# Performance work log

Measured on AMD Instinct MI355X. Metric: run time of the kernel, lower is better.

The kernel has to match this reference:

```python
import jax, jax.numpy as jnp
import numpy as np

B, T, D, H, FF, E = 4, 1024, 1024, 16, 4096, 8
HD = D // H
EPS = 1e-5


def layernorm(x, g, b):
    mu = jnp.mean(x, axis=-1, keepdims=True)
    var = jnp.mean(jnp.square(x - mu), axis=-1, keepdims=True)
    return (x - mu) * jax.lax.rsqrt(var + EPS) * g + b


def setup_inputs() -> dict:
    key = jax.random.key(0)
    ks = jax.random.split(key, 24)
    s = 0.02
    inp = {
        "src": jax.random.normal(ks[0], (B, T, D), jnp.float32),
        "frac": jax.random.uniform(ks[1], (B, T), jnp.float32),
        "Wq": jax.random.normal(ks[2], (D, D), jnp.float32) * s,
        "bq": jnp.zeros((D,), jnp.float32),
        "Wk": jax.random.normal(ks[3], (D, D), jnp.float32) * s,
        "bk": jnp.zeros((D,), jnp.float32),
        "Wv": jax.random.normal(ks[4], (D, D), jnp.float32) * s,
        "bv": jnp.zeros((D,), jnp.float32),
        "Wo": jax.random.normal(ks[5], (D, D), jnp.float32) * s,
        "bo": jnp.zeros((D,), jnp.float32),
        "alpha_pos": jax.random.normal(ks[6], (H,), jnp.float32) * s,
        "alpha_neg": jax.random.normal(ks[7], (H,), jnp.float32) * s,
        "gate_W": jax.random.normal(ks[8], (D, E), jnp.float32) * s,
        "gate_b": jnp.zeros((E,), jnp.float32),
        "W1": jax.random.normal(ks[9], (E, D, FF), jnp.float32) * s,
        "b1": jnp.zeros((E, FF), jnp.float32),
        "W2": jax.random.normal(ks[10], (E, FF, D), jnp.float32) * s,
        "b2": jnp.zeros((E, D), jnp.float32),
        "ln1_g": jnp.ones((D,), jnp.float32),
        "ln1_b": jnp.zeros((D,), jnp.float32),
        "ln2_g": jnp.ones((D,), jnp.float32),
        "ln2_b": jnp.zeros((D,), jnp.float32),
    }
    return inp


def reference(src, frac, Wq, bq, Wk, bk, Wv, bv, Wo, bo, alpha_pos, alpha_neg,
              gate_W, gate_b, W1, b1, W2, b2, ln1_g, ln1_b, ln2_g, ln2_b):
    # ---- attention with per-head stoichiometric bias ----
    q = (src @ Wq + bq).reshape(B, T, H, HD).transpose(0, 2, 1, 3)  # [B,H,T,hd]
    k = (src @ Wk + bk).reshape(B, T, H, HD).transpose(0, 2, 1, 3)
    v = (src @ Wv + bv).reshape(B, T, H, HD).transpose(0, 2, 1, 3)
    scale = HD ** -0.5
    scores = jnp.einsum('bhqd,bhkd->bhqk', q, k) * scale  # [B,H,T,T]
    Dm = frac[:, None, :] - frac[:, :, None]  # frac_j - frac_i, [B,T,T]
    bias = (alpha_pos[None, :, None, None] * jax.nn.relu(Dm)[:, None]
            - alpha_neg[None, :, None, None] * jax.nn.relu(-Dm)[:, None])
    probs = jax.nn.softmax(scores + bias, axis=-1)
    attn = jnp.einsum('bhqk,bhkd->bhqd', probs, v)
    attn = attn.transpose(0, 2, 1, 3).reshape(B, T, D) @ Wo + bo

    x = layernorm(src + attn, ln1_g, ln1_b)

    # ---- top-2 MoE FFN ----
    logits = x @ gate_W + gate_b  # [B,T,E]
    gscores = jax.nn.softmax(logits, axis=-1)
    top2_scores, top2_idx = jax.lax.top_k(gscores, 2)  # [B,T,2]
    # dense per-expert combine weight: score if expert in top-2 else 0
    weights = jnp.sum(jax.nn.one_hot(top2_idx, E, dtype=x.dtype)
                      * top2_scores[..., None], axis=-2)  # [B,T,E]
    ff = jnp.zeros_like(x)
    for e in range(E):  # small fixed expert count
        h = jax.nn.relu(x @ W1[e] + b1[e])
        ff = ff + weights[..., e:e + 1] * (h @ W2[e] + b2[e])

    return layernorm(x + ff, ln2_g, ln2_b)
```

## Files before the change

kernel.cpp:

```cpp
#include <hip/hip_runtime.h>
#include <stdint.h>

typedef unsigned short u16;
typedef unsigned int   u32;

using bf16x8 = __attribute__((ext_vector_type(8))) short;
using f32x4  = __attribute__((ext_vector_type(4))) float;

#define N_T   1024
#define N_D   1024
#define N_E   8
#define N_BT  4096
#define LNEPS 1e-5f

__device__ __forceinline__ u32 rne2(float a, float b) {
  u32 ua = __float_as_uint(a); ua = (ua + 0x7fffu + ((ua >> 16) & 1u)) >> 16;
  u32 ub = __float_as_uint(b); ub = (ub + 0x7fffu + ((ub >> 16) & 1u)) >> 16;
  return ua | (ub << 16);
}
__device__ __forceinline__ u16 rne1(float a) {
  u32 ua = __float_as_uint(a);
  return (u16)((ua + 0x7fffu + ((ua >> 16) & 1u)) >> 16);
}
__device__ __forceinline__ float bfhi_f(float a) {
  u32 ua = __float_as_uint(a);
  ua = (ua + 0x7fffu + ((ua >> 16) & 1u)) & 0xffff0000u;
  return __uint_as_float(ua);
}
__device__ __forceinline__ int fch(int row) { return (row & 3) ^ ((row >> 2) & 3); }
__device__ __forceinline__ int swz(int row, int chunk) {
  return row * 32 + (((chunk ^ fch(row)) & 3) << 3);
}
__device__ __forceinline__ float wred(float v) {
  #pragma unroll
  for (int o2 = 32; o2 > 0; o2 >>= 1) v += __shfl_xor(v, o2, 64);
  return v;
}
__device__ __forceinline__ f32x4 mfma16(bf16x8 a, bf16x8 b, f32x4 c) {
  return __builtin_amdgcn_mfma_f32_16x16x32_bf16(a, b, c, 0, 0, 0);
}
typedef __attribute__((address_space(1))) const u32 gas_u32;
typedef __attribute__((address_space(3))) u32 las_u32;
__device__ __forceinline__ void gl16(const void* g, void* l) {
  __builtin_amdgcn_global_load_lds((gas_u32*)g, (las_u32*)l, 16, 0, 0);
}

template<int SPLIT>
__global__ __launch_bounds__(256)
void transpose_bf16(const float* __restrict__ in, u16* __restrict__ outh,
                    u16* __restrict__ outl, int R, int C, float scale)
{
  __shared__ u16 th[64][68];
  __shared__ u16 tl[SPLIT ? 64 : 1][SPLIT ? 68 : 1];
  const long long zb = (long long)blockIdx.z * R * C;
  const float* srcp = in + zb;
  const int r0 = blockIdx.y * 64, c0 = blockIdx.x * 64;
  const int t = threadIdx.x;
  {
    const int rr = t >> 4, cc = (t & 15) << 2;
    #pragma unroll
    for (int i = 0; i < 4; i++) {
      const int r = rr + i * 16;
      float4 v = *(const float4*)(srcp + (long long)(r0 + r) * C + c0 + cc);
      v.x *= scale; v.y *= scale; v.z *= scale; v.w *= scale;
      if constexpr (SPLIT) {
        float hx = bfhi_f(v.x), hy = bfhi_f(v.y), hz = bfhi_f(v.z), hw = bfhi_f(v.w);
        *(uint2*)&th[r][cc] = make_uint2(rne2(hx, hy), rne2(hz, hw));
        *(uint2*)&tl[r][cc] = make_uint2(rne2(v.x - hx, v.y - hy), rne2(v.z - hz, v.w - hw));
      } else {
        *(uint2*)&th[r][cc] = make_uint2(rne2(v.x, v.y), rne2(v.z, v.w));
      }
    }
  }
  __syncthreads();
  {
    const int c = t >> 2, rs = (t & 3) << 4;
    const long long ob = zb + (long long)(c0 + c) * R + r0 + rs;
    u32 w[8];
    #pragma unroll
    for (int i = 0; i < 8; i++)
      w[i] = (u32)th[rs + 2*i][c] | ((u32)th[rs + 2*i + 1][c] << 16);
    *(uint4*)(outh + ob)     = make_uint4(w[0], w[1], w[2], w[3]);
    *(uint4*)(outh + ob + 8) = make_uint4(w[4], w[5], w[6], w[7]);
    if constexpr (SPLIT) {
      #pragma unroll
      for (int i = 0; i < 8; i++)
        w[i] = (u32)tl[rs + 2*i][c] | ((u32)tl[rs + 2*i + 1][c] << 16);
      *(uint4*)(outl + ob)     = make_uint4(w[0], w[1], w[2], w[3]);
      *(uint4*)(outl + ob + 8) = make_uint4(w[4], w[5], w[6], w[7]);
    }
  }
}

__global__ __launch_bounds__(256)
void bias_cat(const float* __restrict__ bq, const float* __restrict__ bk,
              const float* __restrict__ bv, float* __restrict__ bcat)
{
  const int i = blockIdx.x * 256 + threadIdx.x;
  if (i < 1024)       bcat[i] = bq[i] * 0.125f;
  else if (i < 2048)  bcat[i] = bk[i - 1024];
  else if (i < 3072)  bcat[i] = bv[i - 2048];
}

__global__ __launch_bounds__(256)
void vtrans_bf16(const u16* __restrict__ Vh, const u16* __restrict__ Vl, int ldv,
                 u16* __restrict__ Vth, u16* __restrict__ Vtl)
{
  __shared__ u16 th[64][72];
  __shared__ u16 tl[64][72];
  const int bh = blockIdx.y, b = bh >> 4, h = bh & 15;
  const int kt = blockIdx.x, tid = threadIdx.x;
  {
    const int sr = tid >> 2, scb = (tid & 3) << 4;
    const long long off = (long long)(b * N_T + kt * 64 + sr) * ldv + h * 64 + scb;
    const uint4* vh = (const uint4*)(Vh + off);
    const uint4* vl = (const uint4*)(Vl + off);
    *(uint4*)&th[sr][scb]     = vh[0];
    *(uint4*)&th[sr][scb + 8] = vh[1];
    *(uint4*)&tl[sr][scb]     = vl[0];
    *(uint4*)&tl[sr][scb + 8] = vl[1];
  }
  __syncthreads();
  {
    const int od = tid >> 2, os0 = (tid & 3) << 4;
    u16 wh[16], wl[16];
    #pragma unroll
    for (int i = 0; i < 16; i++) { wh[i] = th[os0 + i][od]; wl[i] = tl[os0 + i][od]; }
    u16* oph = Vth + (long long)(bh * 64 + od) * N_T + kt * 64 + os0;
    u16* opl = Vtl + (long long)(bh * 64 + od) * N_T + kt * 64 + os0;
    *(uint4*)oph = make_uint4((u32)wh[0] | ((u32)wh[1] << 16), (u32)wh[2] | ((u32)wh[3] << 16),
                              (u32)wh[4] | ((u32)wh[5] << 16), (u32)wh[6] | ((u32)wh[7] << 16));
    *(uint4*)(oph + 8) = make_uint4((u32)wh[8] | ((u32)wh[9] << 16), (u32)wh[10] | ((u32)wh[11] << 16),
                                    (u32)wh[12] | ((u32)wh[13] << 16), (u32)wh[14] | ((u32)wh[15] << 16));
    *(uint4*)opl = make_uint4((u32)wl[0] | ((u32)wl[1] << 16), (u32)wl[2] | ((u32)wl[3] << 16),
                              (u32)wl[4] | ((u32)wl[5] << 16), (u32)wl[6] | ((u32)wl[7] << 16));
    *(uint4*)(opl + 8) = make_uint4((u32)wl[8] | ((u32)wl[9] << 16), (u32)wl[10] | ((u32)wl[11] << 16),
                                    (u32)wl[12] | ((u32)wl[13] << 16), (u32)wl[14] | ((u32)wl[15] << 16));
  }
}

template<int ASPLIT, int GATHER, int DORELU, int DOSCALE, int OBF, int GROUPED, int BSPL>
__global__ __launch_bounds__(256, 2)
void gemm128(const void* __restrict__ Ap, int lda,
             const u16* __restrict__ Bhp, const u16* __restrict__ Blp,
             long long bstride,
             void* __restrict__ Cp, int ldc,
             const float* __restrict__ biasp, int bias_stride,
             const float* __restrict__ slot_wp,
             const int* __restrict__ tokidx,
             const int2* __restrict__ tilesp, const int* __restrict__ ntilesp,
             int Ksz, void* __restrict__ Cp2, float cscale)
{
  const int gx = gridDim.x, nwg = gx * gridDim.y;
  const int orig = blockIdx.y * gx + blockIdx.x;
  const int qq = nwg >> 3, rr8 = nwg & 7;
  const int xcd = orig & 7, slot = orig >> 3;
  const int flat = (xcd < rr8 ? xcd * (qq + 1) : rr8 * (qq + 1) + (xcd - rr8) * qq) + slot;
  const int bxx = flat % gx, byy = flat / gx;

  int e = 0, row0;
  if constexpr (GROUPED) {
    if (bxx >= *ntilesp) return;
    const int2 dsc = tilesp[bxx];
    e = dsc.x; row0 = dsc.y;
  } else {
    row0 = bxx * 128;
  }
  const int col0 = byy * 128;

  __shared__ __align__(16) u16 AhS[128 * 32];
  __shared__ __align__(16) u16 BhS[128 * 32];
  __shared__ __align__(16) u16 AlS[ASPLIT ? 128 * 32 : 8];
  __shared__ __align__(16) u16 BlS[BSPL ? 128 * 32 : 8];

  const int tid = threadIdx.x, wid = tid >> 6, lane = tid & 63;
  const int wm = (wid >> 1) << 6, wn = (wid & 1) << 6;
  const int l15 = lane & 15, l4 = lane >> 4;

  const int srow0 = wid * 32 + (lane >> 2);
  const int srow1 = srow0 + 16;
  const int sg0 = ((lane & 3) ^ fch(srow0)) << 3;
  const int sg1 = ((lane & 3) ^ fch(srow1)) << 3;
  u16* lA0 = &AhS[wid * 1024]; u16* lA1 = &AhS[wid * 1024 + 512];
  u16* lB0 = &BhS[wid * 1024]; u16* lB1 = &BhS[wid * 1024 + 512];
  u16* lBl0 = &BlS[(BSPL ? wid : 0) * 1024];
  u16* lBl1 = &BlS[(BSPL ? wid : 0) * 1024 + (BSPL ? 512 : 0)];

  const u16* Bg0 = Bhp + (long long)e * bstride + (long long)(col0 + srow0) * Ksz + sg0;
  const u16* Bg1 = Bhp + (long long)e * bstride + (long long)(col0 + srow1) * Ksz + sg1;
  const u16* Blg0 = nullptr; const u16* Blg1 = nullptr;
  if constexpr (BSPL) {
    Blg0 = Blp + (long long)e * bstride + (long long)(col0 + srow0) * Ksz + sg0;
    Blg1 = Blp + (long long)e * bstride + (long long)(col0 + srow1) * Ksz + sg1;
  }

  const u16* Ag0 = nullptr; const u16* Ag1 = nullptr;
  if constexpr (!ASPLIT) {
    long long ar0, ar1;
    if constexpr (GATHER) { ar0 = tokidx[row0 + srow0]; ar1 = tokidx[row0 + srow1]; }
    else                  { ar0 = row0 + srow0;          ar1 = row0 + srow1; }
    Ag0 = (const u16*)Ap + ar0 * (long long)lda + sg0;
    Ag1 = (const u16*)Ap + ar1 * (long long)lda + sg1;
  }

  const int prr = tid >> 1, pc2 = (tid & 1) << 1;
  const float* Arow = nullptr;
  uint4 sah0, sah1, sal0, sal1;
  if constexpr (ASPLIT) Arow = (const float*)Ap + (long long)(row0 + prr) * lda;

  auto gloadA = [&](int k0) {
    const float4* ap = (const float4*)(Arow + k0 + pc2 * 8);
    float4 f0 = ap[0], f1 = ap[1], f2 = ap[2], f3 = ap[3];
    float h0 = bfhi_f(f0.x), h1 = bfhi_f(f0.y), h2 = bfhi_f(f0.z), h3 = bfhi_f(f0.w);
    float h4 = bfhi_f(f1.x), h5 = bfhi_f(f1.y), h6 = bfhi_f(f1.z), h7 = bfhi_f(f1.w);
    sah0 = make_uint4(rne2(h0, h1), rne2(h2, h3), rne2(h4, h5), rne2(h6, h7));
    sal0 = make_uint4(rne2(f0.x - h0, f0.y - h1), rne2(f0.z - h2, f0.w - h3),
                      rne2(f1.x - h4, f1.y - h5), rne2(f1.z - h6, f1.w - h7));
    h0 = bfhi_f(f2.x); h1 = bfhi_f(f2.y); h2 = bfhi_f(f2.z); h3 = bfhi_f(f2.w);
    h4 = bfhi_f(f3.x); h5 = bfhi_f(f3.y); h6 = bfhi_f(f3.z); h7 = bfhi_f(f3.w);
    sah1 = make_uint4(rne2(h0, h1), rne2(h2, h3), rne2(h4, h5), rne2(h6, h7));
    sal1 = make_uint4(rne2(f2.x - h0, f2.y - h1), rne2(f2.z - h2, f2.w - h3),
                      rne2(f3.x - h4, f3.y - h5), rne2(f3.z - h6, f3.w - h7));
  };

  f32x4 acc[4][4] = {};

  if constexpr (ASPLIT) gloadA(0);
  const int nk = Ksz >> 5;
  for (int kt = 0; kt < nk; kt++) {
    __syncthreads();
    const int ko = kt << 5;
    if constexpr (ASPLIT) {
      *(uint4*)&AhS[swz(prr, pc2)]     = sah0;
      *(uint4*)&AhS[swz(prr, pc2 + 1)] = sah1;
      *(uint4*)&AlS[swz(prr, pc2)]     = sal0;
      *(uint4*)&AlS[swz(prr, pc2 + 1)] = sal1;
    } else {
      gl16(Ag0 + ko, lA0);
      gl16(Ag1 + ko, lA1);
    }
    gl16(Bg0 + ko, lB0);
    gl16(Bg1 + ko, lB1);
    if constexpr (BSPL) {
      gl16(Blg0 + ko, lBl0);
      gl16(Blg1 + ko, lBl1);
    }
    asm volatile("s_waitcnt vmcnt(0)" ::: "memory");
    __syncthreads();
    if constexpr (ASPLIT) if (kt + 1 < nk) gloadA((kt + 1) << 5);

    bf16x8 ah[4], bh[4], al[ASPLIT ? 4 : 1], bl[BSPL ? 4 : 1];
    #pragma unroll
    for (int i = 0; i < 4; i++) {
      const int ar = wm + i * 16 + l15;
      const int br = wn + i * 16 + l15;
      ah[i] = *(const bf16x8*)&AhS[swz(ar, l4)];
      bh[i] = *(const bf16x8*)&BhS[swz(br, l4)];
      if constexpr (ASPLIT) al[i] = *(const bf16x8*)&AlS[swz(ar, l4)];
      if constexpr (BSPL)   bl[i] = *(const bf16x8*)&BlS[swz(br, l4)];
    }
    #pragma unroll
    for (int i = 0; i < 4; i++) {
      #pragma unroll
      for (int j = 0; j < 4; j++) {
        acc[i][j] = mfma16(ah[i], bh[j], acc[i][j]);
        if constexpr (ASPLIT && BSPL) {
          acc[i][j] = mfma16(ah[i], bl[j], acc[i][j]);
          acc[i][j] = mfma16(al[i], bh[j], acc[i][j]);
        }
      }
    }
  }

  #pragma unroll
  for (int i = 0; i < 4; i++) {
    #pragma unroll
    for (int j = 0; j < 4; j++) {
      const int orow0 = row0 + wm + i * 16 + (l4 << 2);
      const int ocol  = col0 + wn + j * 16 + l15;
      const float bv = biasp[(long long)e * bias_stride + col0 + wn + j * 16 + l15];
      #pragma unroll
      for (int q = 0; q < 4; q++) {
        float v = acc[i][j][q] + bv;
        if constexpr (DORELU) v = fmaxf(v, 0.f);
        const long long orow = orow0 + q;
        if constexpr (DOSCALE) v *= slot_wp[orow];
        if constexpr (OBF == 2) {
          const float vs = v * cscale;
          const float hi = bfhi_f(vs);
          ((u16*)Cp )[orow * ldc + ocol] = (u16)(__float_as_uint(hi) >> 16);
          ((u16*)Cp2)[orow * ldc + ocol] = rne1(vs - hi);
        } else if constexpr (OBF == 1) {
          ((u16*)Cp)[orow * ldc + ocol] = rne1(v);
        } else {
          ((float*)Cp)[orow * ldc + ocol] = v;
        }
      }
    }
  }
}

__global__ __launch_bounds__(256, 2)
void attn_mfma(const u16* __restrict__ Qh, const u16* __restrict__ Ql,
               const u16* __restrict__ Kh, const u16* __restrict__ Kl, int ldq,
               const u16* __restrict__ Vth, const u16* __restrict__ Vtl,
               const float* __restrict__ frac,
               const float* __restrict__ apos, const float* __restrict__ aneg,
               float* __restrict__ ctx)
{
  __shared__ __align__(16) u16 KhS[64 * 64];
  __shared__ __align__(16) u16 KlS[64 * 64];
  __shared__ __align__(16) u16 VhS[64 * 64];
  __shared__ __align__(16) u16 VlS[64 * 64];
  __shared__ __align__(16) u16 PS[4][32][72];
  __shared__ __align__(16) float fjS[64];

  const int bh = blockIdx.x, b = bh >> 4, h = bh & 15;
  const int tid = threadIdx.x, wid = tid >> 6, lane = tid & 63;
  const int l15 = lane & 15, l4 = lane >> 4;
  const int q0 = blockIdx.y * 128 + wid * 32;

  bf16x8 qh[2][2], ql[2][2];
  #pragma unroll
  for (int ni = 0; ni < 2; ni++) {
    const long long qoff = (long long)(b * N_T + q0 + ni * 16 + l15) * ldq + h * 64 + l4 * 8;
    #pragma unroll
    for (int ks = 0; ks < 2; ks++) {
      qh[ni][ks] = *(const bf16x8*)(Qh + qoff + ks * 32);
      ql[ni][ks] = *(const bf16x8*)(Ql + qoff + ks * 32);
    }
  }
  float fq[2];
  #pragma unroll
  for (int ni = 0; ni < 2; ni++) fq[ni] = frac[b * N_T + q0 + ni * 16 + l15];
  const float ap = apos[h], an = aneg[h];

  f32x4 acc[4][2] = {};
  float mrun[2] = {-3.0e38f, -3.0e38f}, lrun[2] = {0.f, 0.f};

  const int sr = tid >> 2, scb = (tid & 3) << 4;
  const int ch0 = ((scb >> 3) ^ (sr & 7)) << 3;
  const int ch1 = (((scb >> 3) + 1) ^ (sr & 7)) << 3;

  for (int kt = 0; kt < 16; kt++) {
    __syncthreads();
    {
      const long long koff = (long long)(b * N_T + kt * 64 + sr) * ldq + h * 64 + scb;
      const uint4* khp = (const uint4*)(Kh + koff);
      const uint4* klp = (const uint4*)(Kl + koff);
      const long long voff = (long long)(bh * 64 + sr) * N_T + kt * 64 + scb;
      const uint4* vhp = (const uint4*)(Vth + voff);
      const uint4* vlp = (const uint4*)(Vtl + voff);
      *(uint4*)&KhS[sr * 64 + ch0] = khp[0];
      *(uint4*)&KhS[sr * 64 + ch1] = khp[1];
      *(uint4*)&KlS[sr * 64 + ch0] = klp[0];
      *(uint4*)&KlS[sr * 64 + ch1] = klp[1];
      *(uint4*)&VhS[sr * 64 + ch0] = vhp[0];
      *(uint4*)&VhS[sr * 64 + ch1] = vhp[1];
      *(uint4*)&VlS[sr * 64 + ch0] = vlp[0];
      *(uint4*)&VlS[sr * 64 + ch1] = vlp[1];
    }
    if (tid < 64) fjS[tid] = frac[b * N_T + kt * 64 + tid];
    __syncthreads();

    f32x4 s[4][2] = {};
    #pragma unroll
    for (int ks = 0; ks < 2; ks++) {
      bf16x8 kh[4], kl[4];
      #pragma unroll
      for (int mj = 0; mj < 4; mj++) {
        const int row = mj * 16 + l15;
        const int ch = (((ks << 2) + l4) ^ (row & 7)) << 3;
        kh[mj] = *(const bf16x8*)&KhS[row * 64 + ch];
        kl[mj] = *(const bf16x8*)&KlS[row * 64 + ch];
      }
      #pragma unroll
      for (int mj = 0; mj < 4; mj++) {
        #pragma unroll
        for (int ni = 0; ni < 2; ni++) {
          s[mj][ni] = mfma16(kh[mj], qh[ni][ks], s[mj][ni]);
          s[mj][ni] = mfma16(kh[mj], ql[ni][ks], s[mj][ni]);
          s[mj][ni] = mfma16(kl[mj], qh[ni][ks], s[mj][ni]);
        }
      }
    }

    #pragma unroll
    for (int mj = 0; mj < 4; mj++) {
      const int kvb = mj * 16 + l4 * 4;
      const float f0 = fjS[kvb], f1 = fjS[kvb + 1], f2 = fjS[kvb + 2], f3 = fjS[kvb + 3];
      #pragma unroll
      for (int ni = 0; ni < 2; ni++) {
        float d0 = f0 - fq[ni], d1 = f1 - fq[ni], d2 = f2 - fq[ni], d3 = f3 - fq[ni];
        s[mj][ni][0] += (d0 > 0.f ? ap : an) * d0;
        s[mj][ni][1] += (d1 > 0.f ? ap : an) * d1;
        s[mj][ni][2] += (d2 > 0.f ? ap : an) * d2;
        s[mj][ni][3] += (d3 > 0.f ? ap : an) * d3;
      }
    }

    #pragma unroll
    for (int ni = 0; ni < 2; ni++) {
      float tm = s[0][ni][0];
      #pragma unroll
      for (int mj = 0; mj < 4; mj++) {
        tm = fmaxf(tm, fmaxf(fmaxf(s[mj][ni][0], s[mj][ni][1]),
                             fmaxf(s[mj][ni][2], s[mj][ni][3])));
      }
      tm = fmaxf(tm, __shfl_xor(tm, 16, 64));
      tm = fmaxf(tm, __shfl_xor(tm, 32, 64));
      const float nm = fmaxf(mrun[ni], tm);
      const float cor = __expf(mrun[ni] - nm);
      mrun[ni] = nm;
      lrun[ni] *= cor;
      #pragma unroll
      for (int md = 0; md < 4; md++) {
        acc[md][ni][0] *= cor; acc[md][ni][1] *= cor;
        acc[md][ni][2] *= cor; acc[md][ni][3] *= cor;
      }
      float rsum = 0.f;
      #pragma unroll
      for (int mj = 0; mj < 4; mj++) {
        #pragma unroll
        for (int r = 0; r < 4; r++) {
          const float p = __expf(s[mj][ni][r] - nm);
          s[mj][ni][r] = p;
          rsum += p;
        }
      }
      rsum += __shfl_xor(rsum, 16, 64);
      rsum += __shfl_xor(rsum, 32, 64);
      lrun[ni] += rsum;
    }

    #pragma unroll
    for (int ni = 0; ni < 2; ni++) {
      #pragma unroll
      for (int mj = 0; mj < 4; mj++) {
        float h0 = bfhi_f(s[mj][ni][0]), h1 = bfhi_f(s[mj][ni][1]);
        float h2 = bfhi_f(s[mj][ni][2]), h3 = bfhi_f(s[mj][ni][3]);
        u32* dst = (u32*)&PS[wid][ni * 16 + l15][mj * 16 + l4 * 4];
        dst[0] = rne2(h0, h1); dst[1] = rne2(h2, h3);
      }
    }
    bf16x8 pbh[2][2];
    #pragma unroll
    for (int ni = 0; ni < 2; ni++)
      #pragma unroll
      for (int ks = 0; ks < 2; ks++)
        pbh[ni][ks] = *(const bf16x8*)&PS[wid][ni * 16 + l15][ks * 32 + l4 * 8];

    #pragma unroll
    for (int ni = 0; ni < 2; ni++) {
      #pragma unroll
      for (int mj = 0; mj < 4; mj++) {
        float p0 = s[mj][ni][0], p1 = s[mj][ni][1], p2 = s[mj][ni][2], p3 = s[mj][ni][3];
        float h0 = bfhi_f(p0), h1 = bfhi_f(p1), h2 = bfhi_f(p2), h3 = bfhi_f(p3);
        u32* dst = (u32*)&PS[wid][ni * 16 + l15][mj * 16 + l4 * 4];
        dst[0] = rne2(p0 - h0, p1 - h1); dst[1] = rne2(p2 - h2, p3 - h3);
      }
    }
    bf16x8 pbl[2][2];
    #pragma unroll
    for (int ni = 0; ni < 2; ni++)
      #pragma unroll
      for (int ks = 0; ks < 2; ks++)
        pbl[ni][ks] = *(const bf16x8*)&PS[wid][ni * 16 + l15][ks * 32 + l4 * 8];

    #pragma unroll
    for (int md = 0; md < 4; md++) {
      #pragma unroll
      for (int ks = 0; ks < 2; ks++) {
        const int row = md * 16 + l15;
        const int ch = (((ks << 2) + l4) ^ (row & 7)) << 3;
        const bf16x8 vh = *(const bf16x8*)&VhS[row * 64 + ch];
        const bf16x8 vl = *(const bf16x8*)&VlS[row * 64 + ch];
        #pragma unroll
        for (int nq = 0; nq < 2; nq++) {
          acc[md][nq] = mfma16(vh, pbh[nq][ks], acc[md][nq]);
          acc[md][nq] = mfma16(vh, pbl[nq][ks], acc[md][nq]);
          acc[md][nq] = mfma16(vl, pbh[nq][ks], acc[md][nq]);
        }
      }
    }
  }

  const float inv[2] = {1.f / lrun[0], 1.f / lrun[1]};
  #pragma unroll
  for (int nq = 0; nq < 2; nq++) {
    #pragma unroll
    for (int md = 0; md < 4; md++) {
      float4 o;
      o.x = acc[md][nq][0] * inv[nq];
      o.y = acc[md][nq][1] * inv[nq];
      o.z = acc[md][nq][2] * inv[nq];
      o.w = acc[md][nq][3] * inv[nq];
      *(float4*)(ctx + (long long)(b * N_T + q0 + nq * 16 + l15) * N_D +
                 h * 64 + md * 16 + l4 * 4) = o;
    }
  }
}

__global__ __launch_bounds__(256, 4)
void ln1_gate(const float* __restrict__ src, const float* __restrict__ attnout,
              const float* __restrict__ g, const float* __restrict__ bb,
              const float* __restrict__ gateW, const float* __restrict__ gateb,
              float* __restrict__ xout, u16* __restrict__ xbf,
              int* __restrict__ counts,
              int2* __restrict__ tok_top, float2* __restrict__ tok_w)
{
  const int wid = threadIdx.x >> 6, lane = threadIdx.x & 63;
  const int t = blockIdx.x * 4 + wid;
  const float4* s4 = (const float4*)(src + (long long)t * N_D);
  const float4* a4 = (const float4*)(attnout + (long long)t * N_D);
  float4 v[4];
  float sum = 0.f;
  #pragma unroll
  for (int c = 0; c < 4; c++) {
    const int idx = c * 64 + lane;
    float4 a = s4[idx], b2 = a4[idx];
    v[c] = make_float4(a.x + b2.x, a.y + b2.y, a.z + b2.z, a.w + b2.w);
    sum += v[c].x + v[c].y + v[c].z + v[c].w;
  }
  sum = wred(sum);
  const float mu = sum * (1.f / 1024.f);
  float s2 = 0.f;
  #pragma unroll
  for (int c = 0; c < 4; c++) {
    float dx = v[c].x - mu, dy = v[c].y - mu, dz = v[c].z - mu, dw = v[c].w - mu;
    s2 += dx * dx + dy * dy + dz * dz + dw * dw;
  }
  s2 = wred(s2);
  const float rs = rsqrtf(s2 * (1.f / 1024.f) + LNEPS);
  float acc[8];
  #pragma unroll
  for (int e2 = 0; e2 < 8; e2++) acc[e2] = 0.f;
  #pragma unroll
  for (int c = 0; c < 4; c++) {
    const int idx = c * 64 + lane;
    float4 gv = ((const float4*)g)[idx], bv = ((const float4*)bb)[idx];
    float xa[4];
    xa[0] = (v[c].x - mu) * rs * gv.x + bv.x;
    xa[1] = (v[c].y - mu) * rs * gv.y + bv.y;
    xa[2] = (v[c].z - mu) * rs * gv.z + bv.z;
    xa[3] = (v[c].w - mu) * rs * gv.w + bv.w;
    ((float4*)(xout + (long long)t * N_D))[idx] = make_float4(xa[0], xa[1], xa[2], xa[3]);
    *(uint2*)&xbf[(long long)t * N_D + idx * 4] =
        make_uint2(rne2(xa[0], xa[1]), rne2(xa[2], xa[3]));
    #pragma unroll
    for (int ii = 0; ii < 4; ii++) {
      const float xs = xa[ii];
      const float4* gw = (const float4*)(gateW + ((long long)(idx * 4 + ii)) * N_E);
      float4 w0 = gw[0], w1 = gw[1];
      acc[0] += xs * w0.x; acc[1] += xs * w0.y; acc[2] += xs * w0.z; acc[3] += xs * w0.w;
      acc[4] += xs * w1.x; acc[5] += xs * w1.y; acc[6] += xs * w1.z; acc[7] += xs * w1.w;
    }
  }
  #pragma unroll
  for (int e2 = 0; e2 < 8; e2++) acc[e2] = wred(acc[e2]);
  if (lane == 0) {
    float lg[8];
    #pragma unroll
    for (int e2 = 0; e2 < 8; e2++) lg[e2] = acc[e2] + gateb[e2];
    float mx = lg[0];
    #pragma unroll
    for (int e2 = 1; e2 < 8; e2++) mx = fmaxf(mx, lg[e2]);
    float Z = 0.f;
    #pragma unroll
    for (int e2 = 0; e2 < 8; e2++) Z += __expf(lg[e2] - mx);
    int e0 = 0; float v0 = lg[0];
    #pragma unroll
    for (int e2 = 1; e2 < 8; e2++) if (lg[e2] > v0) { v0 = lg[e2]; e0 = e2; }
    int e1 = -1; float v1 = -3.4e38f;
    #pragma unroll
    for (int e2 = 0; e2 < 8; e2++) if (e2 != e0 && lg[e2] > v1) { v1 = lg[e2]; e1 = e2; }
    atomicAdd(&counts[e0], 1);
    atomicAdd(&counts[e1], 1);
    tok_top[t] = make_int2(e0, e1);
    tok_w[t] = make_float2(__expf(v0 - mx) / Z, __expf(v1 - mx) / Z);
  }
}

__global__ void route_build(const int* __restrict__ counts, int* __restrict__ offsets,
                            int* __restrict__ cursors, int* __restrict__ ntiles,
                            int2* __restrict__ tiles, int* __restrict__ token_idx,
                            float* __restrict__ slot_w)
{
  __shared__ int soff[N_E + 1];
  __shared__ int scnt[N_E];
  if (threadIdx.x == 0) {
    int off = 0, nt = 0;
    for (int ex = 0; ex < N_E; ex++) {
      soff[ex] = off; offsets[ex] = off; cursors[ex] = 0;
      const int cnt = counts[ex];
      scnt[ex] = cnt;
      const int pt = (cnt + 127) >> 7;
      for (int i = 0; i < pt; i++) { tiles[nt] = make_int2(ex, off + i * 128); nt++; }
      off += pt << 7;
    }
    soff[N_E] = off; offsets[N_E] = off;
    *ntiles = nt;
  }
  __syncthreads();
  for (int ex = 0; ex < N_E; ex++)
    for (int s = soff[ex] + scnt[ex] + (int)threadIdx.x; s < soff[ex + 1]; s += (int)blockDim.x) {
      token_idx[s] = 0; slot_w[s] = 0.f;
    }
}

__global__ __launch_bounds__(256)
void route_scatter(const int2* __restrict__ tok_top, const float2* __restrict__ tok_w,
                   const int* __restrict__ offsets, int* __restrict__ cursors,
                   int* __restrict__ token_idx, float* __restrict__ slot_w,
                   int* __restrict__ slotA, int* __restrict__ slotB)
{
  const int t = blockIdx.x * 256 + threadIdx.x;
  if (t >= N_BT) return;
  const int2 ee = tok_top[t];
  const float2 ww = tok_w[t];
  int p = atomicAdd(&cursors[ee.x], 1);
  int s = offsets[ee.x] + p;
  token_idx[s] = t; slot_w[s] = ww.x; slotA[t] = s;
  p = atomicAdd(&cursors[ee.y], 1);
  s = offsets[ee.y] + p;
  token_idx[s] = t; slot_w[s] = ww.y; slotB[t] = s;
}

__global__ __launch_bounds__(256, 4)
void final_ln2(const float* __restrict__ x, const float* __restrict__ out2,
               const int* __restrict__ slotA, const int* __restrict__ slotB,
               const float* __restrict__ g, const float* __restrict__ bb,
               float* __restrict__ out)
{
  const int wid = threadIdx.x >> 6, lane = threadIdx.x & 63;
  const int t = blockIdx.x * 4 + wid;
  const int sA = slotA[t], sB = slotB[t];
  const float4* xr = (const float4*)(x + (long long)t * N_D);
  const float4* pa = (const float4*)(out2 + (long long)sA * N_D);
  const float4* pb = (const float4*)(out2 + (long long)sB * N_D);
  float4 v[4];
  float sum = 0.f;
  #pragma unroll
  for (int c = 0; c < 4; c++) {
    const int idx = c * 64 + lane;
    float4 a = xr[idx], b2 = pa[idx], c2 = pb[idx];
    v[c] = make_float4(a.x + b2.x + c2.x, a.y + b2.y + c2.y,
                       a.z + b2.z + c2.z, a.w + b2.w + c2.w);
    sum += v[c].x + v[c].y + v[c].z + v[c].w;
  }
  sum = wred(sum);
  const float mu = sum * (1.f / 1024.f);
  float s2 = 0.f;
  #pragma unroll
  for (int c = 0; c < 4; c++) {
    float dx = v[c].x - mu, dy = v[c].y - mu, dz = v[c].z - mu, dw = v[c].w - mu;
    s2 += dx * dx + dy * dy + dz * dz + dw * dw;
  }
  s2 = wred(s2);
  const float rs = rsqrtf(s2 * (1.f / 1024.f) + LNEPS);
  #pragma unroll
  for (int c = 0; c < 4; c++) {
    const int idx = c * 64 + lane;
    float4 gv = ((const float4*)g)[idx], bv = ((const float4*)bb)[idx];
    float4 o;
    o.x = (v[c].x - mu) * rs * gv.x + bv.x;
    o.y = (v[c].y - mu) * rs * gv.y + bv.y;
    o.z = (v[c].z - mu) * rs * gv.z + bv.z;
    o.w = (v[c].w - mu) * rs * gv.w + bv.w;
    ((float4*)(out + (long long)t * N_D))[idx] = o;
  }
}

extern "C" void kernel_launch(void* const* d_in, const int* in_sizes, int n_in,
                              void* d_out, int out_size, void* d_ws, size_t ws_size,
                              hipStream_t stream)
{
  const float* src   = (const float*)d_in[0];
  const float* frac  = (const float*)d_in[1];
  const float* Wq    = (const float*)d_in[2];
  const float* bq    = (const float*)d_in[3];
  const float* Wk    = (const float*)d_in[4];
  const float* bk    = (const float*)d_in[5];
  const float* Wv    = (const float*)d_in[6];
  const float* bv    = (const float*)d_in[7];
  const float* Wo    = (const float*)d_in[8];
  const float* bo    = (const float*)d_in[9];
  const float* apos  = (const float*)d_in[10];
  const float* aneg  = (const float*)d_in[11];
  const float* gateW = (const float*)d_in[12];
  const float* gateb = (const float*)d_in[13];
  const float* W1    = (const float*)d_in[14];
  const float* b1    = (const float*)d_in[15];
  const float* W2    = (const float*)d_in[16];
  const float* b2    = (const float*)d_in[17];
  const float* ln1g  = (const float*)d_in[18];
  const float* ln1b  = (const float*)d_in[19];
  const float* ln2g  = (const float*)d_in[20];
  const float* ln2b  = (const float*)d_in[21];
  float* out = (float*)d_out;

  char* ws = (char*)d_ws;
  const size_t MB = 1ull << 20;
  u16* Bcath = (u16*)(ws + 0 * MB);
  u16* Bcatl = (u16*)(ws + 6 * MB);
  u16* WoTh  = (u16*)(ws + 12 * MB);
  u16* WoTl  = (u16*)(ws + 14 * MB);
  u16*   W1T  = (u16*)(ws + 16 * MB);
  float* out2 = (float*)(ws + 16 * MB);
  u16*   W2T  = (u16*)(ws + 80 * MB);
  u16*   QKVh = (u16*)(ws + 144 * MB);
  u16*   QKVl = (u16*)(ws + 168 * MB);
  u16*   Vth  = (u16*)(ws + 192 * MB);
  u16*   Vtl  = (u16*)(ws + 200 * MB);
  float* ctxb = (float*)(ws + 208 * MB);
  float* attnb= (float*)(ws + 144 * MB);
  u16*   hb   = (u16*)(ws + 144 * MB);
  float* xb   = (float*)(ws + 224 * MB);
  u16*   xbf  = (u16*)(ws + 4 * MB);
  float* bcat = (float*)(ws + 240 * MB);
  char* misc = ws + 0;
  int*    counts    = (int*)(misc);
  int*    cursors   = (int*)(misc + 64);
  int*    offsets   = (int*)(misc + 128);
  int*    ntiles    = (int*)(misc + 256);
  int2*   tiles     = (int2*)(misc + 512);
  int2*   tok_top   = (int2*)(misc + 2048);
  float2* tok_w     = (float2*)(misc + 2048 + 32768);
  int*    token_idx = (int*)(misc + 2048 + 65536);
  float*  slot_w    = (float*)(misc + 2048 + 65536 + 36864);
  int*    slotA     = (int*)(misc + 2048 + 65536 + 73728);
  int*    slotB     = (int*)(misc + 2048 + 65536 + 73728 + 16384);

  dim3 b256(256);
  transpose_bf16<1><<<dim3(16, 16, 1), b256, 0, stream>>>(Wq, Bcath, Bcatl,
                                                          1024, 1024, 0.125f);
  transpose_bf16<1><<<dim3(16, 16, 1), b256, 0, stream>>>(Wk, Bcath + 1024 * 1024,
                                                          Bcatl + 1024 * 1024, 1024, 1024, 1.0f);
  transpose_bf16<1><<<dim3(16, 16, 1), b256, 0, stream>>>(Wv, Bcath + 2048 * 1024,
                                                          Bcatl + 2048 * 1024, 1024, 1024, 1.0f);
  transpose_bf16<1><<<dim3(16, 16, 1), b256, 0, stream>>>(Wo, WoTh, WoTl, 1024, 1024, 1.0f);
  transpose_bf16<0><<<dim3(64, 16, 8), b256, 0, stream>>>(W1, W1T, nullptr, 1024, 4096, 1.0f);
  transpose_bf16<0><<<dim3(16, 64, 8), b256, 0, stream>>>(W2, W2T, nullptr, 4096, 1024, 1.0f);
  bias_cat<<<dim3(12), b256, 0, stream>>>(bq, bk, bv, bcat);

  gemm128<1, 0, 0, 0, 2, 0, 1><<<dim3(32, 24), b256, 0, stream>>>(
      src, 1024, Bcath, Bcatl, 0, QKVh, 3072, bcat, 0, nullptr, nullptr, nullptr, nullptr,
      1024, QKVl, 1.0f);

  vtrans_bf16<<<dim3(16, 64), b256, 0, stream>>>(QKVh + 2048, QKVl + 2048, 3072, Vth, Vtl);

  attn_mfma<<<dim3(64, 8), b256, 0, stream>>>(QKVh, QKVl, QKVh + 1024, QKVl + 1024, 3072,
                                              Vth, Vtl, frac, apos, aneg, ctxb);

  gemm128<1, 0, 0, 0, 0, 0, 1><<<dim3(32, 8), b256, 0, stream>>>(
      ctxb, 1024, WoTh, WoTl, 0, attnb, 1024, bo, 0, nullptr, nullptr, nullptr, nullptr,
      1024, nullptr, 1.0f);

  hipMemsetAsync(counts, 0, 32, stream);
  ln1_gate<<<dim3(1024), b256, 0, stream>>>(src, attnb, ln1g, ln1b, gateW, gateb,
                                            xb, xbf, counts, tok_top, tok_w);
  route_build<<<dim3(1), dim3(64), 0, stream>>>(counts, offsets, cursors, ntiles,
                                                tiles, token_idx, slot_w);
  route_scatter<<<dim3(16), b256, 0, stream>>>(tok_top, tok_w, offsets, cursors,
                                               token_idx, slot_w, slotA, slotB);

  gemm128<0, 1, 1, 0, 1, 1, 0><<<dim3(72, 32), b256, 0, stream>>>(
      xbf, 1024, W1T, nullptr, 4096ll * 1024, hb, 4096, b1, 4096,
      nullptr, token_idx, tiles, ntiles, 1024, nullptr, 1.0f);
  gemm128<0, 0, 0, 1, 0, 1, 0><<<dim3(72, 8), b256, 0, stream>>>(
      hb, 4096, W2T, nullptr, 1024ll * 4096, out2, 1024, b2, 1024,
      slot_w, nullptr, tiles, ntiles, 4096, nullptr, 1.0f);

  final_ln2<<<dim3(1024), b256, 0, stream>>>(xb, out2, slotA, slotB, ln2g, ln2b, out);
}
```

Before: 723.6 us.

## Double-buffer LDS in bf16 GEMM path and group tile order by column blocks

For the non-split (bf16 MoE) GEMM, shared-memory A/B tiles are now double-buffered, so the next K-slice's global→LDS loads are issued before the MFMAs on the current slice. This is meant to hide load latency and remove one barrier per iteration. The workgroup-to-tile mapping also changes from XCD-balanced remapping to a simpler XCD stride plus column-grouped ordering (group size CG per launch), aimed at better L2 reuse of weight tiles. The simplified remap assumes the workgroup count is divisible by 8, and the doubled LDS footprint may affect occupancy.

```diff
diff --git a/kernel.cpp b/kernel.cpp
--- a/kernel.cpp
+++ b/kernel.cpp
@@ -139,7 +139,7 @@
   }
 }
 
-template<int ASPLIT, int GATHER, int DORELU, int DOSCALE, int OBF, int GROUPED, int BSPL>
+template<int ASPLIT, int GATHER, int DORELU, int DOSCALE, int OBF, int GROUPED, int CG>
 __global__ __launch_bounds__(256, 2)
 void gemm128(const void* __restrict__ Ap, int lda,
              const u16* __restrict__ Bhp, const u16* __restrict__ Blp,
@@ -153,10 +153,11 @@
 {
   const int gx = gridDim.x, nwg = gx * gridDim.y;
   const int orig = blockIdx.y * gx + blockIdx.x;
-  const int qq = nwg >> 3, rr8 = nwg & 7;
-  const int xcd = orig & 7, slot = orig >> 3;
-  const int flat = (xcd < rr8 ? xcd * (qq + 1) : rr8 * (qq + 1) + (xcd - rr8) * qq) + slot;
-  const int bxx = flat % gx, byy = flat / gx;
+  const int flat = (orig & 7) * (nwg >> 3) + (orig >> 3);
+  const int cgsz = gx * CG;
+  const int colg = flat / cgsz, rem = flat % cgsz;
+  const int bxx = rem / CG;
+  const int byy = colg * CG + rem % CG;
 
   int e = 0, row0;
   if constexpr (GROUPED) {
@@ -168,10 +169,10 @@
   }
   const int col0 = byy * 128;
 
-  __shared__ __align__(16) u16 AhS[128 * 32];
-  __shared__ __align__(16) u16 BhS[128 * 32];
+  __shared__ __align__(16) u16 AhS[ASPLIT ? 1 : 2][128 * 32];
+  __shared__ __align__(16) u16 BhS[ASPLIT ? 1 : 2][128 * 32];
   __shared__ __align__(16) u16 AlS[ASPLIT ? 128 * 32 : 8];
-  __shared__ __align__(16) u16 BlS[BSPL ? 128 * 32 : 8];
+  __shared__ __align__(16) u16 BlS[ASPLIT ? 128 * 32 : 8];
 
   const int tid = threadIdx.x, wid = tid >> 6, lane = tid & 63;
   const int wm = (wid >> 1) << 6, wn = (wid & 1) << 6;
@@ -181,15 +182,12 @@
   const int srow1 = srow0 + 16;
   const int sg0 = ((lane & 3) ^ fch(srow0)) << 3;
   const int sg1 = ((lane & 3) ^ fch(srow1)) << 3;
-  u16* lA0 = &AhS[wid * 1024]; u16* lA1 = &AhS[wid * 1024 + 512];
-  u16* lB0 = &BhS[wid * 1024]; u16* lB1 = &BhS[wid * 1024 + 512];
-  u16* lBl0 = &BlS[(BSPL ? wid : 0) * 1024];
-  u16* lBl1 = &BlS[(BSPL ? wid : 0) * 1024 + (BSPL ? 512 : 0)];
+  const int lo0 = wid * 1024, lo1 = wid * 1024 + 512;
 
   const u16* Bg0 = Bhp + (long long)e * bstride + (long long)(col0 + srow0) * Ksz + sg0;
   const u16* Bg1 = Bhp + (long long)e * bstride + (long long)(col0 + srow1) * Ksz + sg1;
   const u16* Blg0 = nullptr; const u16* Blg1 = nullptr;
-  if constexpr (BSPL) {
+  if constexpr (ASPLIT) {
     Blg0 = Blp + (long long)e * bstride + (long long)(col0 + srow0) * Ksz + sg0;
     Blg1 = Blp + (long long)e * bstride + (long long)(col0 + srow1) * Ksz + sg1;
   }
@@ -203,68 +201,87 @@
     Ag1 = (const u16*)Ap + ar1 * (long long)lda + sg1;
   }
 
-  const int prr = tid >> 1, pc2 = (tid & 1) << 1;
-  const float* Arow = nullptr;
-  uint4 sah0, sah1, sal0, sal1;
-  if constexpr (ASPLIT) Arow = (const float*)Ap + (long long)(row0 + prr) * lda;
-
-  auto gloadA = [&](int k0) {
-    const float4* ap = (const float4*)(Arow + k0 + pc2 * 8);
-    float4 f0 = ap[0], f1 = ap[1], f2 = ap[2], f3 = ap[3];
-    float h0 = bfhi_f(f0.x), h1 = bfhi_f(f0.y), h2 = bfhi_f(f0.z), h3 = bfhi_f(f0.w);
-    float h4 = bfhi_f(f1.x), h5 = bfhi_f(f1.y), h6 = bfhi_f(f1.z), h7 = bfhi_f(f1.w);
-    sah0 = make_uint4(rne2(h0, h1), rne2(h2, h3), rne2(h4, h5), rne2(h6, h7));
-    sal0 = make_uint4(rne2(f0.x - h0, f0.y - h1), rne2(f0.z - h2, f0.w - h3),
-                      rne2(f1.x - h4, f1.y - h5), rne2(f1.z - h6, f1.w - h7));
-    h0 = bfhi_f(f2.x); h1 = bfhi_f(f2.y); h2 = bfhi_f(f2.z); h3 = bfhi_f(f2.w);
-    h4 = bfhi_f(f3.x); h5 = bfhi_f(f3.y); h6 = bfhi_f(f3.z); h7 = bfhi_f(f3.w);
-    sah1 = make_uint4(rne2(h0, h1), rne2(h2, h3), rne2(h4, h5), rne2(h6, h7));
-    sal1 = make_uint4(rne2(f2.x - h0, f2.y - h1), rne2(f2.z - h2, f2.w - h3),
-                      rne2(f3.x - h4, f3.y - h5), rne2(f3.z - h6, f3.w - h7));
-  };
-
   f32x4 acc[4][4] = {};
-
-  if constexpr (ASPLIT) gloadA(0);
   const int nk = Ksz >> 5;
-  for (int kt = 0; kt < nk; kt++) {
-    __syncthreads();
-    const int ko = kt << 5;
-    if constexpr (ASPLIT) {
-      *(uint4*)&AhS[swz(prr, pc2)]     = sah0;
-      *(uint4*)&AhS[swz(prr, pc2 + 1)] = sah1;
-      *(uint4*)&AlS[swz(prr, pc2)]     = sal0;
-      *(uint4*)&AlS[swz(prr, pc2 + 1)] = sal1;
-    } else {
-      gl16(Ag0 + ko, lA0);
-      gl16(Ag1 + ko, lA1);
-    }
-    gl16(Bg0 + ko, lB0);
-    gl16(Bg1 + ko, lB1);
-    if constexpr (BSPL) {
-      gl16(Blg0 + ko, lBl0);
-      gl16(Blg1 + ko, lBl1);
-    }
+
+  if constexpr (!ASPLIT) {
+    gl16(Ag0, &AhS[0][lo0]); gl16(Ag1, &AhS[0][lo1]);
+    gl16(Bg0, &BhS[0][lo0]); gl16(Bg1, &BhS[0][lo1]);
     asm volatile("s_waitcnt vmcnt(0)" ::: "memory");
     __syncthreads();
-    if constexpr (ASPLIT) if (kt + 1 < nk) gloadA((kt + 1) << 5);
-
-    bf16x8 ah[4], bh[4], al[ASPLIT ? 4 : 1], bl[BSPL ? 4 : 1];
-    #pragma unroll
-    for (int i = 0; i < 4; i++) {
-      const int ar = wm + i * 16 + l15;
-      const int br = wn + i * 16 + l15;
-      ah[i] = *(const bf16x8*)&AhS[swz(ar, l4)];
-      bh[i] = *(const bf16x8*)&BhS[swz(br, l4)];
-      if constexpr (ASPLIT) al[i] = *(const bf16x8*)&AlS[swz(ar, l4)];
-      if constexpr (BSPL)   bl[i] = *(const bf16x8*)&BlS[swz(br, l4)];
-    }
-    #pragma unroll
-    for (int i = 0; i < 4; i++) {
-      #pragma unroll
-      for (int j = 0; j < 4; j++) {
-        acc[i][j] = mfma16(ah[i], bh[j], acc[i][j]);
-        if constexpr (ASPLIT && BSPL) {
+    int cur = 0;
+    for (int kt = 0; kt < nk; kt++) {
+      if (kt + 1 < nk) {
+        const int ko = (kt + 1) << 5;
+        gl16(Ag0 + ko, &AhS[cur ^ 1][lo0]);
+        gl16(Ag1 + ko, &AhS[cur ^ 1][lo1]);
+        gl16(Bg0 + ko, &BhS[cur ^ 1][lo0]);
+        gl16(Bg1 + ko, &BhS[cur ^ 1][lo1]);
+      }
+      bf16x8 ah[4], bh[4];
+      #pragma unroll
+      for (int i = 0; i < 4; i++) {
+        ah[i] = *(const bf16x8*)&AhS[cur][swz(wm + i * 16 + l15, l4)];
+        bh[i] = *(const bf16x8*)&BhS[cur][swz(wn + i * 16 + l15, l4)];
+      }
+      #pragma unroll
+      for (int i = 0; i < 4; i++)
+        #pragma unroll
+        for (int j = 0; j < 4; j++)
+          acc[i][j] = mfma16(ah[i], bh[j], acc[i][j]);
+      asm volatile("s_waitcnt vmcnt(0)" ::: "memory");
+      __syncthreads();
+      cur ^= 1;
+    }
+  } else {
+    const int prr = tid >> 1, pc2 = (tid & 1) << 1;
+    const float* Arow = (const float*)Ap + (long long)(row0 + prr) * lda;
+    uint4 sah0, sah1, sal0, sal1;
+    auto gloadA = [&](int k0) {
+      const float4* ap = (const float4*)(Arow + k0 + pc2 * 8);
+      float4 f0 = ap[0], f1 = ap[1], f2 = ap[2], f3 = ap[3];
+      float h0 = bfhi_f(f0.x), h1 = bfhi_f(f0.y), h2 = bfhi_f(f0.z), h3 = bfhi_f(f0.w);
+      float h4 = bfhi_f(f1.x), h5 = bfhi_f(f1.y), h6 = bfhi_f(f1.z), h7 = bfhi_f(f1.w);
+      sah0 = make_uint4(rne2(h0, h1), rne2(h2, h3), rne2(h4, h5), rne2(h6, h7));
+      sal0 = make_uint4(rne2(f0.x - h0, f0.y - h1), rne2(f0.z - h2, f0.w - h3),
+                        rne2(f1.x - h4, f1.y - h5), rne2(f1.z - h6, f1.w - h7));
+      h0 = bfhi_f(f2.x); h1 = bfhi_f(f2.y); h2 = bfhi_f(f2.z); h3 = bfhi_f(f2.w);
+      h4 = bfhi_f(f3.x); h5 = bfhi_f(f3.y); h6 = bfhi_f(f3.z); h7 = bfhi_f(f3.w);
+      sah1 = make_uint4(rne2(h0, h1), rne2(h2, h3), rne2(h4, h5), rne2(h6, h7));
+      sal1 = make_uint4(rne2(f2.x - h0, f2.y - h1), rne2(f2.z - h2, f2.w - h3),
+                        rne2(f3.x - h4, f3.y - h5), rne2(f3.z - h6, f3.w - h7));
+    };
+    gloadA(0);
+    for (int kt = 0; kt < nk; kt++) {
+      __syncthreads();
+      const int ko = kt << 5;
+      *(uint4*)&AhS[0][swz(prr, pc2)]     = sah0;
+      *(uint4*)&AhS[0][swz(prr, pc2 + 1)] = sah1;
+      *(uint4*)&AlS[swz(prr, pc2)]        = sal0;
+      *(uint4*)&AlS[swz(prr, pc2 + 1)]    = sal1;
+      gl16(Bg0 + ko, &BhS[0][lo0]);
+      gl16(Bg1 + ko, &BhS[0][lo1]);
+      gl16(Blg0 + ko, &BlS[lo0]);
+      gl16(Blg1 + ko, &BlS[lo1]);
+      asm volatile("s_waitcnt vmcnt(0)" ::: "memory");
+      __syncthreads();
+      if (kt + 1 < nk) gloadA((kt + 1) << 5);
+
+      bf16x8 ah[4], bh[4], al[4], bl[4];
+      #pragma unroll
+      for (int i = 0; i < 4; i++) {
+        const int ar = wm + i * 16 + l15;
+        const int br = wn + i * 16 + l15;
+        ah[i] = *(const bf16x8*)&AhS[0][swz(ar, l4)];
+        bh[i] = *(const bf16x8*)&BhS[0][swz(br, l4)];
+        al[i] = *(const bf16x8*)&AlS[swz(ar, l4)];
+        bl[i] = *(const bf16x8*)&BlS[swz(br, l4)];
+      }
+      #pragma unroll
+      for (int i = 0; i < 4; i++) {
+        #pragma unroll
+        for (int j = 0; j < 4; j++) {
+          acc[i][j] = mfma16(ah[i], bh[j], acc[i][j]);
           acc[i][j] = mfma16(ah[i], bl[j], acc[i][j]);
           acc[i][j] = mfma16(al[i], bh[j], acc[i][j]);
         }
@@ -743,7 +760,7 @@
   transpose_bf16<0><<<dim3(16, 64, 8), b256, 0, stream>>>(W2, W2T, nullptr, 4096, 1024, 1.0f);
   bias_cat<<<dim3(12), b256, 0, stream>>>(bq, bk, bv, bcat);
 
-  gemm128<1, 0, 0, 0, 2, 0, 1><<<dim3(32, 24), b256, 0, stream>>>(
+  gemm128<1, 0, 0, 0, 2, 0, 3><<<dim3(32, 24), b256, 0, stream>>>(
       src, 1024, Bcath, Bcatl, 0, QKVh, 3072, bcat, 0, nullptr, nullptr, nullptr, nullptr,
       1024, QKVl, 1.0f);
 
@@ -764,10 +781,10 @@
   route_scatter<<<dim3(16), b256, 0, stream>>>(tok_top, tok_w, offsets, cursors,
                                                token_idx, slot_w, slotA, slotB);
 
-  gemm128<0, 1, 1, 0, 1, 1, 0><<<dim3(72, 32), b256, 0, stream>>>(
+  gemm128<0, 1, 1, 0, 1, 1, 4><<<dim3(72, 32), b256, 0, stream>>>(
       xbf, 1024, W1T, nullptr, 4096ll * 1024, hb, 4096, b1, 4096,
       nullptr, token_idx, tiles, ntiles, 1024, nullptr, 1.0f);
-  gemm128<0, 0, 0, 1, 0, 1, 0><<<dim3(72, 8), b256, 0, stream>>>(
+  gemm128<0, 0, 0, 1, 0, 1, 8><<<dim3(72, 8), b256, 0, stream>>>(
       hb, 4096, W2T, nullptr, 1024ll * 4096, out2, 1024, b2, 1024,
       slot_w, nullptr, tiles, ntiles, 4096, nullptr, 1.0f);
 
```

New measurement: 670.1 us. 7.4% less time.
